# Kernel tuning notes

Measured on AMD Instinct MI355X. Metric: run time of the kernel, lower is better.

## Reference

```python
import jax, jax.numpy as jnp
import numpy as np

N_USERS = 50000
N_ITEMS = 50000
N_NODES = N_USERS + N_ITEMS
HID = 128
N_EDGES = 1_600_000


def setup_inputs() -> dict:
    key = jax.random.key(0)
    ks = jax.random.split(key, 10)
    s = 0.02
    return {
        "item": jax.random.randint(ks[0], (N_ITEMS,), 0, N_NODES, dtype=jnp.int32),
        "edge_index": jax.random.randint(ks[1], (2, N_EDGES), 0, N_NODES, dtype=jnp.int32),
        "user_emb": jax.random.normal(ks[2], (N_USERS, HID), jnp.float32) * s,
        "item_emb": jax.random.normal(ks[3], (N_ITEMS, HID), jnp.float32) * s,
        "Wl1": jax.random.normal(ks[4], (HID, HID), jnp.float32) * s,
        "Wr1": jax.random.normal(ks[5], (HID, HID), jnp.float32) * s,
        "b1": jnp.zeros((HID,), jnp.float32),
        "Wl2": jax.random.normal(ks[6], (HID, HID), jnp.float32) * s,
        "Wr2": jax.random.normal(ks[7], (HID, HID), jnp.float32) * s,
        "b2": jnp.zeros((HID,), jnp.float32),
        "W_out": jax.random.normal(ks[8], (HID, 1), jnp.float32) * s,
        "b_out": jnp.zeros((1,), jnp.float32),
        "domain_prior": jnp.ones((1, 1), jnp.float32),
    }


def reference(item, edge_index, user_emb, item_emb, Wl1, Wr1, b1, Wl2, Wr2, b2, W_out, b_out, domain_prior):
    # x = cat(user_embedding.weight, source_item_embedding.weight)  -> [N, HID]
    x = jnp.concatenate([user_emb, item_emb], axis=0)
    n = x.shape[0]
    src, dst = edge_index[0], edge_index[1]
    # mean-aggregation degree (shared across layers; edge structure is fixed)
    deg = jax.ops.segment_sum(jnp.ones(src.shape[0], x.dtype), dst, num_segments=n)
    inv_deg = 1.0 / jnp.maximum(deg, 1.0)  # [N]
    # stacked SAGE convs: out = mean_nbr(x) @ Wl + x @ Wr + b
    for W_l, W_r, b in ((Wl1, Wr1, b1), (Wl2, Wr2, b2)):
        agg = jax.ops.segment_sum(x[src], dst, num_segments=n) * inv_deg[:, None]
        x = agg @ W_l + x @ W_r + b
    item_prior = (x @ W_out + b_out)[item]  # [n_item, 1]
    return jax.nn.relu(domain_prior) * jax.nn.softmax(item_prior, axis=0)
```

## Files before the change

kernel.cpp:

```cpp
#include <hip/hip_runtime.h>
#include <math.h>

#define N_USERS 50000
#define N_ITEMS 50000
#define N_NODES 100000
#define HID     128
#define N_EDGES 1600000

#define BKTW 512
#define NBKT 196
#define NCOL 256
#define EPB  (N_EDGES / NCOL)
#define NH   (NBKT * NCOL)
#define SCAN_H 196

__global__ void k_prep(const float* __restrict__ Wl1, const float* __restrict__ Wr1,
                       const float* __restrict__ b1,  const float* __restrict__ Wl2,
                       const float* __restrict__ Wr2, const float* __restrict__ b2,
                       const float* __restrict__ Wout, const float* __restrict__ bout,
                       float* __restrict__ cvec) {
    __shared__ float w2l[HID], w2r[HID];
    int t = threadIdx.x;
    if (t < 128) {
        float s = 0.f;
        for (int j = 0; j < HID; ++j) s += Wl2[t * HID + j] * Wout[j];
        w2l[t] = s;
    } else {
        int k = t - 128;
        float s = 0.f;
        for (int j = 0; j < HID; ++j) s += Wr2[k * HID + j] * Wout[j];
        w2r[k] = s;
    }
    __syncthreads();
    if (t < 128) {
        float sl = 0.f, sr = 0.f;
        for (int j = 0; j < HID; ++j) {
            float w = Wl1[t * HID + j];
            sl += w * w2l[j];
            sr += w * w2r[j];
        }
        cvec[t]       = sl;
        cvec[256 + t] = sr;
    } else {
        int k = t - 128;
        float sl = 0.f, sr = 0.f;
        for (int j = 0; j < HID; ++j) {
            float w = Wr1[k * HID + j];
            sl += w * w2l[j];
            sr += w * w2r[j];
        }
        cvec[128 + k] = sl;
        cvec[384 + k] = sr;
    }
    if (t == 0) {
        float cl = 0.f;
        for (int j = 0; j < HID; ++j) cl += b1[j] * w2l[j];
        cvec[512] = cl;
    }
    if (t == 1) {
        float cr = 0.f, c = 0.f;
        for (int j = 0; j < HID; ++j) { cr += b1[j] * w2r[j]; c += b2[j] * Wout[j]; }
        cvec[513] = cr + c + bout[0];
    }
}

__global__ __launch_bounds__(256) void k_gemv(const float* __restrict__ ue,
                                              const float* __restrict__ ie,
                                              const float* __restrict__ cvec,
                                              float2* __restrict__ pq,
                                              float2* __restrict__ qq) {
    __shared__ __align__(16) float sc[516];
    int t = threadIdx.x;
    for (int i = t; i < 514; i += 256) sc[i] = cvec[i];
    __syncthreads();
    int g = t >> 4, l = t & 15;
    int n = blockIdx.x * 16 + g;
    const float* x = (n < N_USERS) ? (ue + (size_t)n * HID)
                                   : (ie + (size_t)(n - N_USERS) * HID);
    float4 xa = ((const float4*)x)[2 * l];
    float4 xb = ((const float4*)x)[2 * l + 1];
    const float4* u_l = (const float4*)&sc[0];
    const float4* v_l = (const float4*)&sc[128];
    const float4* u_r = (const float4*)&sc[256];
    const float4* v_r = (const float4*)&sc[384];
    float4 w0, w1;
    w0 = u_l[2 * l]; w1 = u_l[2 * l + 1];
    float pl = xa.x * w0.x + xa.y * w0.y + xa.z * w0.z + xa.w * w0.w
             + xb.x * w1.x + xb.y * w1.y + xb.z * w1.z + xb.w * w1.w;
    w0 = v_l[2 * l]; w1 = v_l[2 * l + 1];
    float ql = xa.x * w0.x + xa.y * w0.y + xa.z * w0.z + xa.w * w0.w
             + xb.x * w1.x + xb.y * w1.y + xb.z * w1.z + xb.w * w1.w;
    w0 = u_r[2 * l]; w1 = u_r[2 * l + 1];
    float pr = xa.x * w0.x + xa.y * w0.y + xa.z * w0.z + xa.w * w0.w
             + xb.x * w1.x + xb.y * w1.y + xb.z * w1.z + xb.w * w1.w;
    w0 = v_r[2 * l]; w1 = v_r[2 * l + 1];
    float qr = xa.x * w0.x + xa.y * w0.y + xa.z * w0.z + xa.w * w0.w
             + xb.x * w1.x + xb.y * w1.y + xb.z * w1.z + xb.w * w1.w;
#pragma unroll
    for (int m = 1; m < 16; m <<= 1) {
        pl += __shfl_xor(pl, m);
        ql += __shfl_xor(ql, m);
        pr += __shfl_xor(pr, m);
        qr += __shfl_xor(qr, m);
    }
    if (l == 0) {
        pq[n] = make_float2(pl, pr);
        qq[n] = make_float2(ql + sc[512], qr + sc[513]);
    }
}

__global__ __launch_bounds__(512) void k_hist(const int* __restrict__ dst,
                                              int* __restrict__ histc) {
    __shared__ int lh[NBKT];
    int t = threadIdx.x, k = blockIdx.x;
    for (int i = t; i < NBKT; i += 512) lh[i] = 0;
    __syncthreads();
    int e0 = k * EPB;
    for (int e = e0 + t; e < e0 + EPB; e += 512)
        atomicAdd(&lh[dst[e] >> 9], 1);
    __syncthreads();
    for (int i = t; i < NBKT; i += 512) histc[i * NCOL + k] = lh[i];
}

__global__ void k_gscan1(const int* __restrict__ in, int* __restrict__ out,
                         int* __restrict__ partials, int n) {
    __shared__ int s[256];
    int t = threadIdx.x;
    int i = blockIdx.x * 256 + t;
    int v = (i < n) ? in[i] : 0;
    s[t] = v;
    __syncthreads();
    for (int off = 1; off < 256; off <<= 1) {
        int add = (t >= off) ? s[t - off] : 0;
        __syncthreads();
        s[t] += add;
        __syncthreads();
    }
    if (i < n) out[i] = s[t] - v;
    if (t == 255) partials[blockIdx.x] = s[255];
}

__global__ void k_scan2(const int* __restrict__ partials, int* __restrict__ poff, int nparts) {
    __shared__ int s[512];
    int t = threadIdx.x;
    int v = (t < nparts) ? partials[t] : 0;
    s[t] = v;
    __syncthreads();
    for (int off = 1; off < 512; off <<= 1) {
        int add = (t >= off) ? s[t - off] : 0;
        __syncthreads();
        s[t] += add;
        __syncthreads();
    }
    poff[t] = s[t] - v;
}

__global__ void k_gscan3(int* __restrict__ out, const int* __restrict__ poff, int n) {
    int i = blockIdx.x * 256 + threadIdx.x;
    if (i < n) out[i] += poff[blockIdx.x];
}

__global__ __launch_bounds__(512) void k_scatA(const int* __restrict__ src,
                                               const int* __restrict__ dst,
                                               const int* __restrict__ hists,
                                               unsigned* __restrict__ part) {
    __shared__ int cur[NBKT];
    int t = threadIdx.x, k = blockIdx.x;
    for (int i = t; i < NBKT; i += 512) cur[i] = hists[i * NCOL + k];
    __syncthreads();
    int e0 = k * EPB;
    for (int e = e0 + t; e < e0 + EPB; e += 512) {
        int s = src[e], d = dst[e];
        int pos = atomicAdd(&cur[d >> 9], 1);
        part[pos] = (unsigned)s | (((unsigned)d & 511u) << 17);
    }
}

__global__ __launch_bounds__(512) void k_aggs1(const unsigned* __restrict__ part,
                                               const int* __restrict__ hists,
                                               const float2* __restrict__ pq,
                                               const float2* __restrict__ qq,
                                               float* __restrict__ zl,
                                               float* __restrict__ zr,
                                               float* __restrict__ invd) {
    __shared__ float suml[BKTW], sumr[BKTW];
    __shared__ int cnt[BKTW];
    int t = threadIdx.x, b = blockIdx.x;
    suml[t] = 0.f; sumr[t] = 0.f; cnt[t] = 0;
    __syncthreads();
    int p0 = hists[b * NCOL];
    int p1 = (b + 1 < NBKT) ? hists[(b + 1) * NCOL] : N_EDGES;
    for (int e = p0 + t; e < p1; e += 512) {
        unsigned enc = part[e];
        float2 p = pq[enc & 0x1FFFFu];
        int dl = enc >> 17;
        atomicAdd(&suml[dl], p.x);
        atomicAdd(&sumr[dl], p.y);
        atomicAdd(&cnt[dl], 1);
    }
    __syncthreads();
    int n = b * BKTW + t;
    if (n < N_NODES) {
        float w = 1.f / (float)max(cnt[t], 1);
        float2 q = qq[n];
        zl[n] = suml[t] * w + q.x;
        zr[n] = sumr[t] * w + q.y;
        invd[n] = w;
    }
}

__global__ __launch_bounds__(512) void k_aggs2(const unsigned* __restrict__ part,
                                               const int* __restrict__ hists,
                                               const float* __restrict__ zl,
                                               const float* __restrict__ zr,
                                               const float* __restrict__ invd,
                                               float* __restrict__ y) {
    __shared__ float sum[BKTW];
    int t = threadIdx.x, b = blockIdx.x;
    sum[t] = 0.f;
    __syncthreads();
    int p0 = hists[b * NCOL];
    int p1 = (b + 1 < NBKT) ? hists[(b + 1) * NCOL] : N_EDGES;
    for (int e = p0 + t; e < p1; e += 512) {
        unsigned enc = part[e];
        atomicAdd(&sum[enc >> 17], zl[enc & 0x1FFFFu]);
    }
    __syncthreads();
    int n = b * BKTW + t;
    if (n < N_NODES) y[n] = sum[t] * invd[n] + zr[n];
}

__global__ void k_sumexp(const float* __restrict__ y, const int* __restrict__ item,
                         float* __restrict__ redsum) {
    float s = 0.f;
    for (int i = blockIdx.x * blockDim.x + threadIdx.x; i < N_ITEMS; i += gridDim.x * blockDim.x)
        s += expf(y[item[i]]);
#pragma unroll
    for (int off = 32; off; off >>= 1) s += __shfl_down(s, off, 64);
    __shared__ float sm[4];
    int lane = threadIdx.x & 63, wave = threadIdx.x >> 6;
    if (lane == 0) sm[wave] = s;
    __syncthreads();
    if (threadIdx.x == 0) atomicAdd(redsum, sm[0] + sm[1] + sm[2] + sm[3]);
}

__global__ void k_out(const float* __restrict__ y, const int* __restrict__ item,
                      const float* __restrict__ redsum, const float* __restrict__ dprior,
                      float* __restrict__ out) {
    float inv_s = 1.0f / (*redsum);
    float pr = fmaxf(dprior[0], 0.f);
    for (int i = blockIdx.x * blockDim.x + threadIdx.x; i < N_ITEMS; i += gridDim.x * blockDim.x)
        out[i] = pr * expf(y[item[i]]) * inv_s;
}

extern "C" void kernel_launch(void* const* d_in, const int* in_sizes, int n_in,
                              void* d_out, int out_size, void* d_ws, size_t ws_size,
                              hipStream_t stream) {
    const int*   item  = (const int*)d_in[0];
    const int*   esrc  = (const int*)d_in[1];
    const int*   edst  = esrc + N_EDGES;
    const float* ue    = (const float*)d_in[2];
    const float* ie    = (const float*)d_in[3];
    const float* Wl1   = (const float*)d_in[4];
    const float* Wr1   = (const float*)d_in[5];
    const float* b1    = (const float*)d_in[6];
    const float* Wl2   = (const float*)d_in[7];
    const float* Wr2   = (const float*)d_in[8];
    const float* b2    = (const float*)d_in[9];
    const float* Wout  = (const float*)d_in[10];
    const float* bout  = (const float*)d_in[11];
    const float* dpri  = (const float*)d_in[12];
    float* out = (float*)d_out;

    unsigned* part = (unsigned*)d_ws;
    float2*   pq   = (float2*)(part + N_EDGES);
    float2*   qq   = pq + N_NODES;
    float*    zl   = (float*)(qq + N_NODES);
    float*    zr   = zl + N_NODES;
    float*    invd = zr + N_NODES;
    float*    y    = invd + N_NODES;
    int*      histc   = (int*)(y + N_NODES);
    int*      hists   = histc + NH;
    int*      parts_h = hists + NH;
    int*      poff_h  = parts_h + 512;
    float*    cvec    = (float*)(poff_h + 512);
    float*    redsum  = cvec + 516;

    hipMemsetAsync((void*)redsum, 0, 4, stream);

    k_prep<<<1, 256, 0, stream>>>(Wl1, Wr1, b1, Wl2, Wr2, b2, Wout, bout, cvec);
    k_gemv<<<N_NODES / 16, 256, 0, stream>>>(ue, ie, cvec, pq, qq);

    k_hist<<<NCOL, 512, 0, stream>>>(edst, histc);
    k_gscan1<<<SCAN_H, 256, 0, stream>>>(histc, hists, parts_h, NH);
    k_scan2<<<1, 512, 0, stream>>>(parts_h, poff_h, SCAN_H);
    k_gscan3<<<SCAN_H, 256, 0, stream>>>(hists, poff_h, NH);
    k_scatA<<<NCOL, 512, 0, stream>>>(esrc, edst, hists, part);

    k_aggs1<<<NBKT, 512, 0, stream>>>(part, hists, pq, qq, zl, zr, invd);
    k_aggs2<<<NBKT, 512, 0, stream>>>(part, hists, zl, zr, invd, y);

    k_sumexp<<<200, 256, 0, stream>>>(y, item, redsum);
    k_out<<<200, 256, 0, stream>>>(y, item, redsum, dpri, out);
}
```

Measured before the change: 206.7 us.

## Fuse histogram into GEMV launch, merge scan passes, privatize LDS atomics per wave

The edge histogram now runs as extra blocks appended to the GEMV grid, with per-wave private LDS histograms. The three-pass scan becomes two kernels, with each block re-scanning the partials itself, and the redsum memset moves into the prep kernel. The aggregation kernels now give each wave its own LDS accumulator copy to cut atomic contention, at the cost of 8x more shared memory and a final reduction. Together these drop several launches and reduce same-address LDS atomic conflicts.

```diff
diff --git a/kernel.cpp b/kernel.cpp
--- a/kernel.cpp
+++ b/kernel.cpp
@@ -13,12 +13,13 @@
 #define EPB  (N_EDGES / NCOL)
 #define NH   (NBKT * NCOL)
 #define SCAN_H 196
+#define GEMV_BLKS (N_NODES / 16)
 
 __global__ void k_prep(const float* __restrict__ Wl1, const float* __restrict__ Wr1,
                        const float* __restrict__ b1,  const float* __restrict__ Wl2,
                        const float* __restrict__ Wr2, const float* __restrict__ b2,
                        const float* __restrict__ Wout, const float* __restrict__ bout,
-                       float* __restrict__ cvec) {
+                       float* __restrict__ cvec, float* __restrict__ redsum) {
     __shared__ float w2l[HID], w2r[HID];
     int t = threadIdx.x;
     if (t < 128) {
@@ -62,15 +63,32 @@
         for (int j = 0; j < HID; ++j) { cr += b1[j] * w2r[j]; c += b2[j] * Wout[j]; }
         cvec[513] = cr + c + bout[0];
     }
-}
-
-__global__ __launch_bounds__(256) void k_gemv(const float* __restrict__ ue,
-                                              const float* __restrict__ ie,
-                                              const float* __restrict__ cvec,
-                                              float2* __restrict__ pq,
-                                              float2* __restrict__ qq) {
-    __shared__ __align__(16) float sc[516];
+    if (t == 2) *redsum = 0.f;
+}
+
+__global__ __launch_bounds__(256) void k_gemvhist(const float* __restrict__ ue,
+                                                  const float* __restrict__ ie,
+                                                  const float* __restrict__ cvec,
+                                                  float2* __restrict__ pq,
+                                                  float2* __restrict__ qq,
+                                                  const int* __restrict__ dst,
+                                                  int* __restrict__ histc) {
+    __shared__ __align__(16) float sc[4 * NBKT];
     int t = threadIdx.x;
+    if (blockIdx.x >= GEMV_BLKS) {
+        int* lh = (int*)sc;
+        int k = blockIdx.x - GEMV_BLKS;
+        for (int i = t; i < 4 * NBKT; i += 256) lh[i] = 0;
+        __syncthreads();
+        int* mylh = lh + (t >> 6) * NBKT;
+        int e0 = k * EPB;
+        for (int e = e0 + t; e < e0 + EPB; e += 256)
+            atomicAdd(&mylh[dst[e] >> 9], 1);
+        __syncthreads();
+        for (int i = t; i < NBKT; i += 256)
+            histc[i * NCOL + k] = lh[i] + lh[NBKT + i] + lh[2 * NBKT + i] + lh[3 * NBKT + i];
+        return;
+    }
     for (int i = t; i < 514; i += 256) sc[i] = cvec[i];
     __syncthreads();
     int g = t >> 4, l = t & 15;
@@ -109,25 +127,12 @@
     }
 }
 
-__global__ __launch_bounds__(512) void k_hist(const int* __restrict__ dst,
-                                              int* __restrict__ histc) {
-    __shared__ int lh[NBKT];
-    int t = threadIdx.x, k = blockIdx.x;
-    for (int i = t; i < NBKT; i += 512) lh[i] = 0;
-    __syncthreads();
-    int e0 = k * EPB;
-    for (int e = e0 + t; e < e0 + EPB; e += 512)
-        atomicAdd(&lh[dst[e] >> 9], 1);
-    __syncthreads();
-    for (int i = t; i < NBKT; i += 512) histc[i * NCOL + k] = lh[i];
-}
-
-__global__ void k_gscan1(const int* __restrict__ in, int* __restrict__ out,
-                         int* __restrict__ partials, int n) {
+__global__ void k_scanA(const int* __restrict__ in, int* __restrict__ out,
+                        int* __restrict__ partials) {
     __shared__ int s[256];
     int t = threadIdx.x;
     int i = blockIdx.x * 256 + t;
-    int v = (i < n) ? in[i] : 0;
+    int v = in[i];
     s[t] = v;
     __syncthreads();
     for (int off = 1; off < 256; off <<= 1) {
@@ -136,28 +141,24 @@
         s[t] += add;
         __syncthreads();
     }
-    if (i < n) out[i] = s[t] - v;
+    out[i] = s[t] - v;
     if (t == 255) partials[blockIdx.x] = s[255];
 }
 
-__global__ void k_scan2(const int* __restrict__ partials, int* __restrict__ poff, int nparts) {
-    __shared__ int s[512];
-    int t = threadIdx.x;
-    int v = (t < nparts) ? partials[t] : 0;
+__global__ void k_scanB(int* __restrict__ out, const int* __restrict__ partials) {
+    __shared__ int s[256];
+    int t = threadIdx.x, b = blockIdx.x;
+    int v = (t < SCAN_H) ? partials[t] : 0;
     s[t] = v;
     __syncthreads();
-    for (int off = 1; off < 512; off <<= 1) {
+    for (int off = 1; off < 256; off <<= 1) {
         int add = (t >= off) ? s[t - off] : 0;
         __syncthreads();
         s[t] += add;
         __syncthreads();
     }
-    poff[t] = s[t] - v;
-}
-
-__global__ void k_gscan3(int* __restrict__ out, const int* __restrict__ poff, int n) {
-    int i = blockIdx.x * 256 + threadIdx.x;
-    if (i < n) out[i] += poff[blockIdx.x];
+    int off = s[b] - partials[b];
+    out[b * 256 + t] += off;
 }
 
 __global__ __launch_bounds__(512) void k_scatA(const int* __restrict__ src,
@@ -183,29 +184,47 @@
                                                float* __restrict__ zl,
                                                float* __restrict__ zr,
                                                float* __restrict__ invd) {
-    __shared__ float suml[BKTW], sumr[BKTW];
-    __shared__ int cnt[BKTW];
+    __shared__ float suml[8 * BKTW];
+    __shared__ float sumr[8 * BKTW];
+    __shared__ int   cnt[8 * BKTW];
     int t = threadIdx.x, b = blockIdx.x;
-    suml[t] = 0.f; sumr[t] = 0.f; cnt[t] = 0;
-    __syncthreads();
+    int w = t >> 6;
+#pragma unroll
+    for (int i = 0; i < 8; ++i) {
+        suml[t + i * 512] = 0.f;
+        sumr[t + i * 512] = 0.f;
+        cnt[t + i * 512] = 0;
+    }
+    __syncthreads();
+    float* msl = suml + w * BKTW;
+    float* msr = sumr + w * BKTW;
+    int*   mc  = cnt + w * BKTW;
     int p0 = hists[b * NCOL];
     int p1 = (b + 1 < NBKT) ? hists[(b + 1) * NCOL] : N_EDGES;
     for (int e = p0 + t; e < p1; e += 512) {
         unsigned enc = part[e];
         float2 p = pq[enc & 0x1FFFFu];
         int dl = enc >> 17;
-        atomicAdd(&suml[dl], p.x);
-        atomicAdd(&sumr[dl], p.y);
-        atomicAdd(&cnt[dl], 1);
-    }
-    __syncthreads();
+        atomicAdd(&msl[dl], p.x);
+        atomicAdd(&msr[dl], p.y);
+        atomicAdd(&mc[dl], 1);
+    }
+    __syncthreads();
+    float sl = 0.f, sr = 0.f;
+    int c = 0;
+#pragma unroll
+    for (int i = 0; i < 8; ++i) {
+        sl += suml[i * BKTW + t];
+        sr += sumr[i * BKTW + t];
+        c += cnt[i * BKTW + t];
+    }
     int n = b * BKTW + t;
     if (n < N_NODES) {
-        float w = 1.f / (float)max(cnt[t], 1);
+        float wi = 1.f / (float)max(c, 1);
         float2 q = qq[n];
-        zl[n] = suml[t] * w + q.x;
-        zr[n] = sumr[t] * w + q.y;
-        invd[n] = w;
+        zl[n] = sl * wi + q.x;
+        zr[n] = sr * wi + q.y;
+        invd[n] = wi;
     }
 }
 
@@ -215,19 +234,25 @@
                                                const float* __restrict__ zr,
                                                const float* __restrict__ invd,
                                                float* __restrict__ y) {
-    __shared__ float sum[BKTW];
+    __shared__ float sum[8 * BKTW];
     int t = threadIdx.x, b = blockIdx.x;
-    sum[t] = 0.f;
-    __syncthreads();
+    int w = t >> 6;
+#pragma unroll
+    for (int i = 0; i < 8; ++i) sum[t + i * 512] = 0.f;
+    __syncthreads();
+    float* ms = sum + w * BKTW;
     int p0 = hists[b * NCOL];
     int p1 = (b + 1 < NBKT) ? hists[(b + 1) * NCOL] : N_EDGES;
     for (int e = p0 + t; e < p1; e += 512) {
         unsigned enc = part[e];
-        atomicAdd(&sum[enc >> 17], zl[enc & 0x1FFFFu]);
-    }
-    __syncthreads();
+        atomicAdd(&ms[enc >> 17], zl[enc & 0x1FFFFu]);
+    }
+    __syncthreads();
+    float s = 0.f;
+#pragma unroll
+    for (int i = 0; i < 8; ++i) s += sum[i * BKTW + t];
     int n = b * BKTW + t;
-    if (n < N_NODES) y[n] = sum[t] * invd[n] + zr[n];
+    if (n < N_NODES) y[n] = s * invd[n] + zr[n];
 }
 
 __global__ void k_sumexp(const float* __restrict__ y, const int* __restrict__ item,
@@ -282,19 +307,15 @@
     int*      histc   = (int*)(y + N_NODES);
     int*      hists   = histc + NH;
     int*      parts_h = hists + NH;
-    int*      poff_h  = parts_h + 512;
-    float*    cvec    = (float*)(poff_h + 512);
+    float*    cvec    = (float*)(parts_h + 512);
     float*    redsum  = cvec + 516;
 
-    hipMemsetAsync((void*)redsum, 0, 4, stream);
-
-    k_prep<<<1, 256, 0, stream>>>(Wl1, Wr1, b1, Wl2, Wr2, b2, Wout, bout, cvec);
-    k_gemv<<<N_NODES / 16, 256, 0, stream>>>(ue, ie, cvec, pq, qq);
-
-    k_hist<<<NCOL, 512, 0, stream>>>(edst, histc);
-    k_gscan1<<<SCAN_H, 256, 0, stream>>>(histc, hists, parts_h, NH);
-    k_scan2<<<1, 512, 0, stream>>>(parts_h, poff_h, SCAN_H);
-    k_gscan3<<<SCAN_H, 256, 0, stream>>>(hists, poff_h, NH);
+    k_prep<<<1, 256, 0, stream>>>(Wl1, Wr1, b1, Wl2, Wr2, b2, Wout, bout, cvec, redsum);
+    k_gemvhist<<<GEMV_BLKS + NCOL, 256, 0, stream>>>(ue, ie, cvec, pq, qq, edst, histc);
+
+    k_scanA<<<SCAN_H, 256, 0, stream>>>(histc, hists, parts_h);
+    k_scanB<<<SCAN_H, 256, 0, stream>>>(hists, parts_h);
+
     k_scatA<<<NCOL, 512, 0, stream>>>(esrc, edst, hists, part);
 
     k_aggs1<<<NBKT, 512, 0, stream>>>(part, hists, pq, qq, zl, zr, invd);
```

New measurement: 208.2 us. About the same (+0.7%).
